# Optimization experiments

Measured on AMD Instinct MI355X. Metric: run time of the kernel, lower is better.

Reference implementation:

```python
import jax, jax.numpy as jnp
import numpy as np

EMBED_DIM = 512
NUM_HEADS = 8
HEAD_DIM = EMBED_DIM // NUM_HEADS


def setup_inputs() -> dict:
    key = jax.random.key(0)
    ks = jax.random.split(key, 6)
    B, S, D = 2, 4096, EMBED_DIM
    scale = 1.0 / np.sqrt(D)
    inputs = jax.random.normal(ks[0], (B, S, D), dtype=jnp.float32)
    Wq = jax.random.normal(ks[1], (D, D), dtype=jnp.float32) * scale
    Wk = jax.random.normal(ks[2], (D, D), dtype=jnp.float32) * scale
    Wv = jax.random.normal(ks[3], (D, D), dtype=jnp.float32) * scale
    Wo = jax.random.normal(ks[4], (D, D), dtype=jnp.float32) * scale
    zeros = jnp.zeros((D,), dtype=jnp.float32)
    return {"inputs": inputs, "Wq": Wq, "bq": zeros, "Wk": Wk, "bk": zeros,
            "Wv": Wv, "bv": zeros, "Wo": Wo, "bo": zeros}


def _split_heads(x, B, S):
    # [B,S,D] -> [B,H,S,hd]
    return x.reshape(B, S, NUM_HEADS, HEAD_DIM).transpose(0, 2, 1, 3)


def reference(inputs, Wq, bq, Wk, bk, Wv, bv, Wo, bo):
    B, S, D = inputs.shape
    q = _split_heads(inputs @ Wq + bq, B, S)
    k = _split_heads(inputs @ Wk + bk, B, S)
    v = _split_heads(inputs @ Wv + bv, B, S)
    scale = 1.0 / jnp.sqrt(jnp.asarray(HEAD_DIM, dtype=inputs.dtype))
    # full [B,H,S,S] score matrix, as in the original naive SDPA
    scores = jnp.einsum('bhqd,bhkd->bhqk', q, k) * scale
    weights = jax.nn.softmax(scores, axis=-1)
    attn = jnp.einsum('bhqk,bhkd->bhqd', weights, v)
    attn = attn.transpose(0, 2, 1, 3).reshape(B, S, D)
    return attn @ Wo + bo
```

## Files before the change

kernel.cpp:

```cpp
#include <hip/hip_runtime.h>
#include <hip/hip_bf16.h>
#include <stdint.h>


typedef __bf16 bf16x8 __attribute__((ext_vector_type(8)));
typedef float f32x4 __attribute__((ext_vector_type(4)));
typedef float f32x16 __attribute__((ext_vector_type(16)));

using as1_void = __attribute__((address_space(1))) void;
using as3_void = __attribute__((address_space(3))) void;

__device__ __forceinline__ void gload16(const void* g, void* l) {
    __builtin_amdgcn_global_load_lds((const as1_void*)g, (as3_void*)l, 16, 0, 0);
}

__device__ __forceinline__ f32x4 mfma16(bf16x8 a, bf16x8 b, f32x4 c) {
    return __builtin_amdgcn_mfma_f32_16x16x32_bf16(a, b, c, 0, 0, 0);
}

__device__ __forceinline__ f32x16 mfma32(bf16x8 a, bf16x8 b, f32x16 c) {
    return __builtin_amdgcn_mfma_f32_32x32x16_bf16(a, b, c, 0, 0, 0);
}

__device__ __forceinline__ uint32_t pkbf(float a, float b) {
    union { __hip_bfloat16 h[2]; uint32_t u; } r;
    r.h[0] = __float2bfloat16(a);
    r.h[1] = __float2bfloat16(b);
    return r.u;
}

__device__ __forceinline__ void pl32swap(uint32_t& a, uint32_t& b) {
#if __has_builtin(__builtin_amdgcn_permlane32_swap)
    typedef unsigned int uint32x2_t __attribute__((ext_vector_type(2)));
    uint32x2_t r = __builtin_amdgcn_permlane32_swap(a, b, false, false);
    a = r[0];
    b = r[1];
#else
    asm volatile("v_permlane32_swap_b32 %0, %1" : "+v"(a), "+v"(b));
#endif
}

__global__ void cvt_all(const float* __restrict__ X, __hip_bfloat16* __restrict__ Xb,
                        const float* __restrict__ w0, const float* __restrict__ w1,
                        const float* __restrict__ w2, const float* __restrict__ w3,
                        __hip_bfloat16* __restrict__ o0, __hip_bfloat16* __restrict__ o1,
                        __hip_bfloat16* __restrict__ o2, __hip_bfloat16* __restrict__ o3) {
    __shared__ float t[32][33];
    const int bid = blockIdx.x, tid = threadIdx.x;
    if (bid < 1024) {
        const float* W; __hip_bfloat16* O;
        switch (bid >> 8) {
            case 0: W = w0; O = o0; break;
            case 1: W = w1; O = o1; break;
            case 2: W = w2; O = o2; break;
            default: W = w3; O = o3; break;
        }
        int rem = bid & 255;
        int n0 = (rem & 15) * 32, k0 = (rem >> 4) * 32;
        int tx = tid & 31, ty = tid >> 5;
        for (int j = 0; j < 4; ++j)
            t[ty + 8 * j][tx] = W[(size_t)(k0 + ty + 8 * j) * 512 + n0 + tx];
        __syncthreads();
        for (int j = 0; j < 4; ++j)
            O[(size_t)(n0 + ty + 8 * j) * 512 + k0 + tx] = __float2bfloat16(t[tx][ty + 8 * j]);
    } else {
        int i = ((bid - 1024) * 256 + tid) * 4;
        float4 v = *reinterpret_cast<const float4*>(X + i);
        uint2 u;
        u.x = pkbf(v.x, v.y);
        u.y = pkbf(v.z, v.w);
        *reinterpret_cast<uint2*>(Xb + i) = u;
    }
}

__global__ __launch_bounds__(256, 2) void gemm_qkv(
    const __hip_bfloat16* __restrict__ A, const __hip_bfloat16* __restrict__ Bt,
    const float* __restrict__ bq, const float* __restrict__ bk, const float* __restrict__ bv,
    __hip_bfloat16* __restrict__ Qb, __hip_bfloat16* __restrict__ Kb,
    __hip_bfloat16* __restrict__ Vtb, float qs)
{
    const int K = 512;
    __shared__ __hip_bfloat16 Abuf[128 * 32];
    __shared__ __hip_bfloat16 Bbuf[128 * 32];
    const int tid = threadIdx.x, w = tid >> 6, lane = tid & 63;
    const int col = lane & 15, quad = lane >> 4;
    const int wr = w >> 1, wc = w & 1;
    const int tileN = blockIdx.x * 128, tileM = blockIdx.y * 128;

    f32x4 acc[4][4] = {};

    for (int k0 = 0; k0 < K; k0 += 32) {
        for (int i = 0; i < 2; ++i) {
            int g = w * 2 + i;
            int chunk = g * 64 + lane;
            int row = chunk >> 2, c8 = chunk & 3;
            gload16(A + (size_t)(tileM + row) * K + k0 + c8 * 8, Abuf + g * 512);
            gload16(Bt + (size_t)(tileN + row) * K + k0 + c8 * 8, Bbuf + g * 512);
        }
        __syncthreads();
        bf16x8 af[4], bfr[4];
        for (int mt = 0; mt < 4; ++mt)
            af[mt] = *reinterpret_cast<const bf16x8*>(Abuf + (wr * 64 + mt * 16 + col) * 32 + quad * 8);
        for (int nt = 0; nt < 4; ++nt)
            bfr[nt] = *reinterpret_cast<const bf16x8*>(Bbuf + (wc * 64 + nt * 16 + col) * 32 + quad * 8);
        for (int mt = 0; mt < 4; ++mt)
            for (int nt = 0; nt < 4; ++nt)
                acc[mt][nt] = mfma16(af[mt], bfr[nt], acc[mt][nt]);
        __syncthreads();
    }

    const int seg = (tileN + wc * 64) >> 9;
    const float* bias = (seg == 0) ? bq : (seg == 1) ? bk : bv;
    const float scale = (seg == 0) ? qs : 1.0f;
    __hip_bfloat16* outp = (seg == 0) ? Qb : (seg == 1) ? Kb : Vtb;

    for (int mt = 0; mt < 4; ++mt) {
        for (int nt = 0; nt < 4; ++nt) {
            int n = tileN + wc * 64 + nt * 16 + col;
            int nn = n & 511, h = nn >> 6, d = nn & 63;
            float bn = bias[nn];
            for (int r = 0; r < 4; ++r) {
                int m = tileM + wr * 64 + mt * 16 + quad * 4 + r;
                int b = m >> 12, s = m & 4095;
                float v = (acc[mt][nt][r] + bn) * scale;
                size_t off;
                if (seg < 2) off = (((size_t)(b * 8 + h) * 4096 + s) << 6) + d;
                else         off = (((size_t)(b * 8 + h) * 64 + d) << 12) + s;
                outp[off] = __float2bfloat16(v);
            }
        }
    }
}

__global__ __launch_bounds__(256, 2) void gemm_out(
    const __hip_bfloat16* __restrict__ A, const __hip_bfloat16* __restrict__ Bt,
    const float* __restrict__ bias, float* __restrict__ out)
{
    const int N = 512, K = 512;
    __shared__ __hip_bfloat16 Abuf[128 * 32];
    __shared__ __hip_bfloat16 Bbuf[64 * 32];
    const int tid = threadIdx.x, w = tid >> 6, lane = tid & 63;
    const int col = lane & 15, quad = lane >> 4;
    const int tileN = blockIdx.x * 64, tileM = blockIdx.y * 128;

    f32x4 acc[2][4] = {};

    for (int k0 = 0; k0 < K; k0 += 32) {
        for (int i = 0; i < 2; ++i) {
            int g = w * 2 + i;
            int chunk = g * 64 + lane;
            int row = chunk >> 2, c8 = chunk & 3;
            gload16(A + (size_t)(tileM + row) * K + k0 + c8 * 8, Abuf + g * 512);
        }
        {
            int row = tid >> 2, c8 = tid & 3;
            gload16(Bt + (size_t)(tileN + row) * K + k0 + c8 * 8, Bbuf + tid * 8);
        }
        __syncthreads();
        bf16x8 af[2], bfr[4];
        for (int mt = 0; mt < 2; ++mt)
            af[mt] = *reinterpret_cast<const bf16x8*>(Abuf + (w * 32 + mt * 16 + col) * 32 + quad * 8);
        for (int nt = 0; nt < 4; ++nt)
            bfr[nt] = *reinterpret_cast<const bf16x8*>(Bbuf + (nt * 16 + col) * 32 + quad * 8);
        for (int mt = 0; mt < 2; ++mt)
            for (int nt = 0; nt < 4; ++nt)
                acc[mt][nt] = mfma16(af[mt], bfr[nt], acc[mt][nt]);
        __syncthreads();
    }

    for (int mt = 0; mt < 2; ++mt) {
        for (int nt = 0; nt < 4; ++nt) {
            int n = tileN + nt * 16 + col;
            float bn = bias[n];
            for (int r = 0; r < 4; ++r) {
                int m = tileM + w * 32 + mt * 16 + quad * 4 + r;
                out[(size_t)m * N + n] = acc[mt][nt][r] + bn;
            }
        }
    }
}

__global__ __launch_bounds__(256, 2) void flash(
    const __hip_bfloat16* __restrict__ Q,
    const __hip_bfloat16* __restrict__ Kq,
    const __hip_bfloat16* __restrict__ Vt,
    __hip_bfloat16* __restrict__ O1,
    __hip_bfloat16* __restrict__ O2,
    float* __restrict__ Lb)
{
    __shared__ __hip_bfloat16 KT[2][4096];
    __shared__ __hip_bfloat16 VB[2][4096];

    const int bh = blockIdx.y, b = bh >> 3, hq = bh & 7;
    const int kvh = blockIdx.z;
    const int base = kvh * 32;
    const int tid = threadIdx.x, w = tid >> 6, lane = tid & 63;
    const int l31 = lane & 31, hh = lane >> 5, l7 = lane & 7;
    const int q0 = blockIdx.x * 128 + w * 32;

    const __hip_bfloat16* Qh = Q + (size_t)bh * 4096 * 64;
    const __hip_bfloat16* Kh = Kq + (size_t)bh * 4096 * 64;
    const __hip_bfloat16* Vh = Vt + (size_t)bh * 64 * 4096;

    bf16x8 aq[4];
#pragma unroll
    for (int dk = 0; dk < 4; ++dk)
        aq[dk] = *reinterpret_cast<const bf16x8*>(
            Qh + (size_t)(q0 + l31) * 64 + dk * 16 + hh * 8);

    const __hip_bfloat16* ksrc[2];
    const __hip_bfloat16* vsrc[2];
    int ldsoff[2];
#pragma unroll
    for (int i = 0; i < 2; ++i) {
        int c = i * 256 + tid;
        int row = c >> 3, s8 = (c & 7) ^ (row & 7);
        ksrc[i] = Kh + row * 64 + s8 * 8;
        vsrc[i] = Vh + (size_t)row * 4096 + s8 * 8;
        ldsoff[i] = (i * 256 + w * 64) * 8;
    }

    bf16x8 ones;
#pragma unroll
    for (int j = 0; j < 8; ++j) ones[j] = (__bf16)1.0f;

    const f32x16 z16 = {};
    f32x16 o[2] = {};
    f32x16 lacc = {};
    f32x16 sc[2][2];

    gload16(ksrc[0] + (size_t)base * 4096, &KT[0][ldsoff[0]]);
    gload16(ksrc[1] + (size_t)base * 4096, &KT[0][ldsoff[1]]);
    gload16(vsrc[0] + (size_t)base * 64, &VB[0][ldsoff[0]]);
    gload16(vsrc[1] + (size_t)base * 64, &VB[0][ldsoff[1]]);
    gload16(ksrc[0] + (size_t)(base + 1) * 4096, &KT[1][ldsoff[0]]);
    gload16(ksrc[1] + (size_t)(base + 1) * 4096, &KT[1][ldsoff[1]]);
    __syncthreads();

#define QK_STEP(KR_, SP2_)                                                      \
    _Pragma("unroll")                                                           \
    for (int kg = 0; kg < 2; ++kg) {                                            \
        _Pragma("unroll")                                                       \
        for (int dk = 0; dk < 4; ++dk) {                                        \
            bf16x8 ak = *reinterpret_cast<const bf16x8*>(                       \
                &KT[KR_][(kg * 32 + l31) * 64 + (((dk * 2 + hh) ^ l7) << 3)]);  \
            sc[SP2_][kg] = (dk == 0) ? mfma32(ak, aq[0], z16)                   \
                                     : mfma32(ak, aq[dk], sc[SP2_][kg]);        \
        }                                                                       \
    }

#define SOFTMAX_EXCHANGE(SP_)                                                   \
    uint32_t U[8][2];                                                           \
    _Pragma("unroll")                                                           \
    for (int kg = 0; kg < 2; ++kg) {                                            \
        f32x16 v = sc[SP_][kg];                                                 \
        _Pragma("unroll")                                                       \
        for (int rr = 0; rr < 4; ++rr) {                                        \
            U[kg * 4 + rr][0] = pkbf(__builtin_amdgcn_exp2f(v[rr * 4 + 0]),     \
                                     __builtin_amdgcn_exp2f(v[rr * 4 + 1]));    \
            U[kg * 4 + rr][1] = pkbf(__builtin_amdgcn_exp2f(v[rr * 4 + 2]),     \
                                     __builtin_amdgcn_exp2f(v[rr * 4 + 3]));    \
        }                                                                       \
    }                                                                           \
    bf16x8 bp[4];                                                               \
    _Pragma("unroll")                                                           \
    for (int kb = 0; kb < 4; ++kb) {                                            \
        _Pragma("unroll")                                                       \
        for (int t2 = 0; t2 < 2; ++t2)                                          \
            pl32swap(U[2 * kb][t2], U[2 * kb + 1][t2]);                         \
        union { uint32_t u[4]; bf16x8 v8; } cc;                                 \
        cc.u[0] = U[2 * kb][0];     cc.u[1] = U[2 * kb][1];                     \
        cc.u[2] = U[2 * kb + 1][0]; cc.u[3] = U[2 * kb + 1][1];                 \
        bp[kb] = cc.v8;                                                         \
    }

#define PV_STEP(VR_)                                                            \
    _Pragma("unroll")                                                           \
    for (int dg = 0; dg < 2; ++dg) {                                            \
        _Pragma("unroll")                                                       \
        for (int kb = 0; kb < 4; ++kb) {                                        \
            bf16x8 av = *reinterpret_cast<const bf16x8*>(                       \
                &VB[VR_][(dg * 32 + l31) * 64 + (((kb * 2 + hh) ^ l7) << 3)]);  \
            o[dg] = mfma32(av, bp[kb], o[dg]);                                  \
        }                                                                       \
    }                                                                           \
    _Pragma("unroll")                                                           \
    for (int kb = 0; kb < 4; ++kb) lacc = mfma32(ones, bp[kb], lacc);

    QK_STEP(0, 0)
    __syncthreads();

#define FLASH_BODY(T_, P_)                                                      \
    {                                                                           \
        const int kt_ = (T_);                                                   \
        int kk = kt_ + 2; if (kk > base + 31) kk = base + 31;                   \
        gload16(ksrc[0] + (size_t)kk * 4096, &KT[(P_)][ldsoff[0]]);             \
        gload16(ksrc[1] + (size_t)kk * 4096, &KT[(P_)][ldsoff[1]]);             \
        gload16(vsrc[0] + (size_t)(kt_ + 1) * 64, &VB[1 - (P_)][ldsoff[0]]);    \
        gload16(vsrc[1] + (size_t)(kt_ + 1) * 64, &VB[1 - (P_)][ldsoff[1]]);    \
        SOFTMAX_EXCHANGE(P_)                                                    \
        QK_STEP(1 - (P_), 1 - (P_))                                             \
        PV_STEP(P_)                                                             \
        __syncthreads();                                                        \
    }

    FLASH_BODY(base + 0, 0)
    for (int kth = 0; kth < 15; ++kth) {
        FLASH_BODY(base + 2 * kth + 1, 1)
        FLASH_BODY(base + 2 * kth + 2, 0)
    }
    {
        SOFTMAX_EXCHANGE(1)
        PV_STEP(1)
    }
#undef FLASH_BODY
#undef PV_STEP
#undef SOFTMAX_EXCHANGE
#undef QK_STEP

    {
        float l = lacc[0];
        float inv = 1.0f / l;
        int s = q0 + l31;
        __hip_bfloat16* Od = kvh ? O2 : O1;
        __hip_bfloat16* dst = Od + ((size_t)b * 4096 + s) * 512 + hq * 64;
#pragma unroll
        for (int dg = 0; dg < 2; ++dg)
#pragma unroll
            for (int rr = 0; rr < 4; ++rr) {
                uint2 u;
                u.x = pkbf(o[dg][rr * 4 + 0] * inv, o[dg][rr * 4 + 1] * inv);
                u.y = pkbf(o[dg][rr * 4 + 2] * inv, o[dg][rr * 4 + 3] * inv);
                *reinterpret_cast<uint2*>(dst + dg * 32 + rr * 8 + hh * 4) = u;
            }
        if (hh == 0)
            Lb[((size_t)kvh * 16 + bh) * 4096 + s] = l;
    }
}

__global__ __launch_bounds__(256) void merge_po(
    const __hip_bfloat16* __restrict__ O1, const __hip_bfloat16* __restrict__ O2,
    const float* __restrict__ Lb, __hip_bfloat16* __restrict__ Am)
{
    int c = blockIdx.x * 256 + threadIdx.x;
    int flat = c * 8;
    int d = flat & 511, s = (flat >> 9) & 4095, b = flat >> 21;
    int bh = b * 8 + (d >> 6);
    float l1 = Lb[(size_t)bh * 4096 + s];
    float l2 = Lb[(size_t)(16 + bh) * 4096 + s];
    float rs = 1.0f / (l1 + l2);
    float w1 = l1 * rs, w2 = l2 * rs;
    bf16x8 a = *reinterpret_cast<const bf16x8*>(O1 + flat);
    bf16x8 bb = *reinterpret_cast<const bf16x8*>(O2 + flat);
    uint2 u;
    float r0 = w1 * (float)a[0] + w2 * (float)bb[0];
    float r1 = w1 * (float)a[1] + w2 * (float)bb[1];
    float r2 = w1 * (float)a[2] + w2 * (float)bb[2];
    float r3 = w1 * (float)a[3] + w2 * (float)bb[3];
    float r4 = w1 * (float)a[4] + w2 * (float)bb[4];
    float r5 = w1 * (float)a[5] + w2 * (float)bb[5];
    float r6 = w1 * (float)a[6] + w2 * (float)bb[6];
    float r7 = w1 * (float)a[7] + w2 * (float)bb[7];
    u.x = pkbf(r0, r1);
    u.y = pkbf(r2, r3);
    uint2 v;
    v.x = pkbf(r4, r5);
    v.y = pkbf(r6, r7);
    uint4 uu = {u.x, u.y, v.x, v.y};
    *reinterpret_cast<uint4*>(Am + flat) = uu;
}

extern "C" void kernel_launch(void* const* d_in, const int* in_sizes, int n_in,
                              void* d_out, int out_size, void* d_ws, size_t ws_size,
                              hipStream_t stream) {
    const float* X  = (const float*)d_in[0];
    const float* Wq = (const float*)d_in[1];
    const float* bq = (const float*)d_in[2];
    const float* Wk = (const float*)d_in[3];
    const float* bk = (const float*)d_in[4];
    const float* Wv = (const float*)d_in[5];
    const float* bv = (const float*)d_in[6];
    const float* Wo = (const float*)d_in[7];
    const float* bo = (const float*)d_in[8];
    float* out = (float*)d_out;

    char* ws = (char*)d_ws;
    __hip_bfloat16* Xb  = (__hip_bfloat16*)(ws);
    __hip_bfloat16* Wqt = (__hip_bfloat16*)(ws + ((size_t)8 << 20));
    __hip_bfloat16* Wkt = Wqt + 512 * 512;
    __hip_bfloat16* Wvt = Wkt + 512 * 512;
    __hip_bfloat16* Wot = Wvt + 512 * 512;
    __hip_bfloat16* Qb  = (__hip_bfloat16*)(ws + ((size_t)10 << 20));
    __hip_bfloat16* Kb  = (__hip_bfloat16*)(ws + ((size_t)18 << 20));
    __hip_bfloat16* Vtb = (__hip_bfloat16*)(ws + ((size_t)26 << 20));
    __hip_bfloat16* O1  = (__hip_bfloat16*)(ws + ((size_t)34 << 20));
    __hip_bfloat16* O2  = (__hip_bfloat16*)(ws);
    __hip_bfloat16* Am  = (__hip_bfloat16*)(ws + ((size_t)10 << 20));
    float* Lb = (float*)d_out;

    cvt_all<<<5120, 256, 0, stream>>>(X, Xb, Wq, Wk, Wv, Wo, Wqt, Wkt, Wvt, Wot);

    const float qs = 0.125f * 1.4426950408889634f;
    gemm_qkv<<<dim3(12, 64), 256, 0, stream>>>(Xb, Wqt, bq, bk, bv, Qb, Kb, Vtb, qs);
    flash<<<dim3(32, 16, 2), 256, 0, stream>>>(Qb, Kb, Vtb, O1, O2, Lb);
    merge_po<<<2048, 256, 0, stream>>>(O1, O2, Lb, Am);
    gemm_out<<<dim3(8, 64), 256, 0, stream>>>(Am, Wot, bo, out);
}
```

Baseline: 221.2 us.

## Give each flash wave two query tiles and compute row sums on VALU

```diff
diff --git a/kernel.cpp b/kernel.cpp
--- a/kernel.cpp
+++ b/kernel.cpp
@@ -180,7 +180,7 @@
     }
 }
 
-__global__ __launch_bounds__(256, 2) void flash(
+__global__ __launch_bounds__(128, 2) void flash(
     const __hip_bfloat16* __restrict__ Q,
     const __hip_bfloat16* __restrict__ Kq,
     const __hip_bfloat16* __restrict__ Vt,
@@ -196,82 +196,93 @@
     const int base = kvh * 32;
     const int tid = threadIdx.x, w = tid >> 6, lane = tid & 63;
     const int l31 = lane & 31, hh = lane >> 5, l7 = lane & 7;
-    const int q0 = blockIdx.x * 128 + w * 32;
+    const int q0 = blockIdx.x * 128 + w * 64;
 
     const __hip_bfloat16* Qh = Q + (size_t)bh * 4096 * 64;
     const __hip_bfloat16* Kh = Kq + (size_t)bh * 4096 * 64;
     const __hip_bfloat16* Vh = Vt + (size_t)bh * 64 * 4096;
 
-    bf16x8 aq[4];
-#pragma unroll
-    for (int dk = 0; dk < 4; ++dk)
-        aq[dk] = *reinterpret_cast<const bf16x8*>(
-            Qh + (size_t)(q0 + l31) * 64 + dk * 16 + hh * 8);
-
-    const __hip_bfloat16* ksrc[2];
-    const __hip_bfloat16* vsrc[2];
-    int ldsoff[2];
-#pragma unroll
-    for (int i = 0; i < 2; ++i) {
-        int c = i * 256 + tid;
+    bf16x8 aq[2][4];
+#pragma unroll
+    for (int qg = 0; qg < 2; ++qg)
+#pragma unroll
+        for (int dk = 0; dk < 4; ++dk)
+            aq[qg][dk] = *reinterpret_cast<const bf16x8*>(
+                Qh + (size_t)(q0 + qg * 32 + l31) * 64 + dk * 16 + hh * 8);
+
+    const __hip_bfloat16* ksrc[4];
+    const __hip_bfloat16* vsrc[4];
+    int ldsoff[4];
+#pragma unroll
+    for (int i = 0; i < 4; ++i) {
+        int c = i * 128 + tid;
         int row = c >> 3, s8 = (c & 7) ^ (row & 7);
         ksrc[i] = Kh + row * 64 + s8 * 8;
         vsrc[i] = Vh + (size_t)row * 4096 + s8 * 8;
-        ldsoff[i] = (i * 256 + w * 64) * 8;
-    }
-
-    bf16x8 ones;
-#pragma unroll
-    for (int j = 0; j < 8; ++j) ones[j] = (__bf16)1.0f;
+        ldsoff[i] = (i * 128 + w * 64) * 8;
+    }
 
     const f32x16 z16 = {};
-    f32x16 o[2] = {};
-    f32x16 lacc = {};
+    f32x16 o[2][2] = {};
     f32x16 sc[2][2];
-
-    gload16(ksrc[0] + (size_t)base * 4096, &KT[0][ldsoff[0]]);
-    gload16(ksrc[1] + (size_t)base * 4096, &KT[0][ldsoff[1]]);
-    gload16(vsrc[0] + (size_t)base * 64, &VB[0][ldsoff[0]]);
-    gload16(vsrc[1] + (size_t)base * 64, &VB[0][ldsoff[1]]);
-    gload16(ksrc[0] + (size_t)(base + 1) * 4096, &KT[1][ldsoff[0]]);
-    gload16(ksrc[1] + (size_t)(base + 1) * 4096, &KT[1][ldsoff[1]]);
+    float ltot[2] = {0.f, 0.f};
+
+#pragma unroll
+    for (int i = 0; i < 4; ++i) gload16(ksrc[i] + (size_t)base * 4096, &KT[0][ldsoff[i]]);
+#pragma unroll
+    for (int i = 0; i < 4; ++i) gload16(vsrc[i] + (size_t)base * 64, &VB[0][ldsoff[i]]);
+#pragma unroll
+    for (int i = 0; i < 4; ++i) gload16(ksrc[i] + (size_t)(base + 1) * 4096, &KT[1][ldsoff[i]]);
     __syncthreads();
 
-#define QK_STEP(KR_, SP2_)                                                      \
+#define QK_STEP(KR_)                                                            \
     _Pragma("unroll")                                                           \
     for (int kg = 0; kg < 2; ++kg) {                                            \
         _Pragma("unroll")                                                       \
         for (int dk = 0; dk < 4; ++dk) {                                        \
             bf16x8 ak = *reinterpret_cast<const bf16x8*>(                       \
                 &KT[KR_][(kg * 32 + l31) * 64 + (((dk * 2 + hh) ^ l7) << 3)]);  \
-            sc[SP2_][kg] = (dk == 0) ? mfma32(ak, aq[0], z16)                   \
-                                     : mfma32(ak, aq[dk], sc[SP2_][kg]);        \
+            _Pragma("unroll")                                                   \
+            for (int qg = 0; qg < 2; ++qg)                                      \
+                sc[qg][kg] = (dk == 0) ? mfma32(ak, aq[qg][0], z16)             \
+                                       : mfma32(ak, aq[qg][dk], sc[qg][kg]);    \
         }                                                                       \
     }
 
-#define SOFTMAX_EXCHANGE(SP_)                                                   \
-    uint32_t U[8][2];                                                           \
+#define SOFTMAX_BP()                                                            \
+    bf16x8 bp[2][4];                                                            \
     _Pragma("unroll")                                                           \
-    for (int kg = 0; kg < 2; ++kg) {                                            \
-        f32x16 v = sc[SP_][kg];                                                 \
-        _Pragma("unroll")                                                       \
-        for (int rr = 0; rr < 4; ++rr) {                                        \
-            U[kg * 4 + rr][0] = pkbf(__builtin_amdgcn_exp2f(v[rr * 4 + 0]),     \
-                                     __builtin_amdgcn_exp2f(v[rr * 4 + 1]));    \
-            U[kg * 4 + rr][1] = pkbf(__builtin_amdgcn_exp2f(v[rr * 4 + 2]),     \
-                                     __builtin_amdgcn_exp2f(v[rr * 4 + 3]));    \
+    for (int qg = 0; qg < 2; ++qg) {                                            \
+        float ls = 0.f;                                                         \
+        uint32_t U[8][2];                                                       \
+        _Pragma("unroll")                                                       \
+        for (int kg = 0; kg < 2; ++kg) {                                        \
+            f32x16 v = sc[qg][kg];                                              \
+            _Pragma("unroll")                                                   \
+            for (int rr = 0; rr < 4; ++rr) {                                    \
+                float e0 = __builtin_amdgcn_exp2f(v[rr * 4 + 0]);               \
+                float e1 = __builtin_amdgcn_exp2f(v[rr * 4 + 1]);               \
+                float e2 = __builtin_amdgcn_exp2f(v[rr * 4 + 2]);               \
+                float e3 = __builtin_amdgcn_exp2f(v[rr * 4 + 3]);               \
+                ls += (e0 + e1) + (e2 + e3);                                    \
+                U[kg * 4 + rr][0] = pkbf(e0, e1);                               \
+                U[kg * 4 + rr][1] = pkbf(e2, e3);                               \
+            }                                                                   \
         }                                                                       \
-    }                                                                           \
-    bf16x8 bp[4];                                                               \
-    _Pragma("unroll")                                                           \
-    for (int kb = 0; kb < 4; ++kb) {                                            \
-        _Pragma("unroll")                                                       \
-        for (int t2 = 0; t2 < 2; ++t2)                                          \
-            pl32swap(U[2 * kb][t2], U[2 * kb + 1][t2]);                         \
-        union { uint32_t u[4]; bf16x8 v8; } cc;                                 \
-        cc.u[0] = U[2 * kb][0];     cc.u[1] = U[2 * kb][1];                     \
-        cc.u[2] = U[2 * kb + 1][0]; cc.u[3] = U[2 * kb + 1][1];                 \
-        bp[kb] = cc.v8;                                                         \
+        union fu_ { float f; uint32_t u; };                                     \
+        fu_ la, lb2;                                                            \
+        la.f = ls; lb2.u = la.u;                                                \
+        pl32swap(la.u, lb2.u);                                                  \
+        ltot[qg] += la.f + lb2.f;                                               \
+        _Pragma("unroll")                                                       \
+        for (int kb = 0; kb < 4; ++kb) {                                        \
+            pl32swap(U[2 * kb][0], U[2 * kb + 1][0]);                           \
+            pl32swap(U[2 * kb][1], U[2 * kb + 1][1]);                           \
+            union { uint32_t u[4]; bf16x8 v8; } cc;                             \
+            cc.u[0] = U[2 * kb][0];     cc.u[1] = U[2 * kb][1];                 \
+            cc.u[2] = U[2 * kb + 1][0]; cc.u[3] = U[2 * kb + 1][1];             \
+            bp[qg][kb] = cc.v8;                                                 \
+        }                                                                       \
     }
 
 #define PV_STEP(VR_)                                                            \
@@ -281,25 +292,27 @@
         for (int kb = 0; kb < 4; ++kb) {                                        \
             bf16x8 av = *reinterpret_cast<const bf16x8*>(                       \
                 &VB[VR_][(dg * 32 + l31) * 64 + (((kb * 2 + hh) ^ l7) << 3)]);  \
-            o[dg] = mfma32(av, bp[kb], o[dg]);                                  \
+            _Pragma("unroll")                                                   \
+            for (int qg = 0; qg < 2; ++qg)                                      \
+                o[qg][dg] = mfma32(av, bp[qg][kb], o[qg][dg]);                  \
         }                                                                       \
-    }                                                                           \
-    _Pragma("unroll")                                                           \
-    for (int kb = 0; kb < 4; ++kb) lacc = mfma32(ones, bp[kb], lacc);
-
-    QK_STEP(0, 0)
+    }
+
+    QK_STEP(0)
     __syncthreads();
 
 #define FLASH_BODY(T_, P_)                                                      \
     {                                                                           \
         const int kt_ = (T_);                                                   \
         int kk = kt_ + 2; if (kk > base + 31) kk = base + 31;                   \
-        gload16(ksrc[0] + (size_t)kk * 4096, &KT[(P_)][ldsoff[0]]);             \
-        gload16(ksrc[1] + (size_t)kk * 4096, &KT[(P_)][ldsoff[1]]);             \
-        gload16(vsrc[0] + (size_t)(kt_ + 1) * 64, &VB[1 - (P_)][ldsoff[0]]);    \
-        gload16(vsrc[1] + (size_t)(kt_ + 1) * 64, &VB[1 - (P_)][ldsoff[1]]);    \
-        SOFTMAX_EXCHANGE(P_)                                                    \
-        QK_STEP(1 - (P_), 1 - (P_))                                             \
+        _Pragma("unroll")                                                       \
+        for (int i = 0; i < 4; ++i)                                             \
+            gload16(ksrc[i] + (size_t)kk * 4096, &KT[(P_)][ldsoff[i]]);         \
+        _Pragma("unroll")                                                       \
+        for (int i = 0; i < 4; ++i)                                             \
+            gload16(vsrc[i] + (size_t)(kt_ + 1) * 64, &VB[1 - (P_)][ldsoff[i]]);\
+        SOFTMAX_BP()                                                            \
+        QK_STEP(1 - (P_))                                                       \
         PV_STEP(P_)                                                             \
         __syncthreads();                                                        \
     }
@@ -310,18 +323,19 @@
         FLASH_BODY(base + 2 * kth + 2, 0)
     }
     {
-        SOFTMAX_EXCHANGE(1)
+        SOFTMAX_BP()
         PV_STEP(1)
     }
 #undef FLASH_BODY
 #undef PV_STEP
-#undef SOFTMAX_EXCHANGE
+#undef SOFTMAX_BP
 #undef QK_STEP
 
-    {
-        float l = lacc[0];
+#pragma unroll
+    for (int qg = 0; qg < 2; ++qg) {
+        float l = ltot[qg];
         float inv = 1.0f / l;
-        int s = q0 + l31;
+        int s = q0 + qg * 32 + l31;
         __hip_bfloat16* Od = kvh ? O2 : O1;
         __hip_bfloat16* dst = Od + ((size_t)b * 4096 + s) * 512 + hq * 64;
 #pragma unroll
@@ -329,8 +343,8 @@
 #pragma unroll
             for (int rr = 0; rr < 4; ++rr) {
                 uint2 u;
-                u.x = pkbf(o[dg][rr * 4 + 0] * inv, o[dg][rr * 4 + 1] * inv);
-                u.y = pkbf(o[dg][rr * 4 + 2] * inv, o[dg][rr * 4 + 3] * inv);
+                u.x = pkbf(o[qg][dg][rr * 4 + 0] * inv, o[qg][dg][rr * 4 + 1] * inv);
+                u.y = pkbf(o[qg][dg][rr * 4 + 2] * inv, o[qg][dg][rr * 4 + 3] * inv);
                 *reinterpret_cast<uint2*>(dst + dg * 32 + rr * 8 + hh * 4) = u;
             }
         if (hh == 0)
@@ -352,7 +366,6 @@
     float w1 = l1 * rs, w2 = l2 * rs;
     bf16x8 a = *reinterpret_cast<const bf16x8*>(O1 + flat);
     bf16x8 bb = *reinterpret_cast<const bf16x8*>(O2 + flat);
-    uint2 u;
     float r0 = w1 * (float)a[0] + w2 * (float)bb[0];
     float r1 = w1 * (float)a[1] + w2 * (float)bb[1];
     float r2 = w1 * (float)a[2] + w2 * (float)bb[2];
@@ -361,12 +374,11 @@
     float r5 = w1 * (float)a[5] + w2 * (float)bb[5];
     float r6 = w1 * (float)a[6] + w2 * (float)bb[6];
     float r7 = w1 * (float)a[7] + w2 * (float)bb[7];
-    u.x = pkbf(r0, r1);
-    u.y = pkbf(r2, r3);
-    uint2 v;
-    v.x = pkbf(r4, r5);
-    v.y = pkbf(r6, r7);
-    uint4 uu = {u.x, u.y, v.x, v.y};
+    uint4 uu;
+    uu.x = pkbf(r0, r1);
+    uu.y = pkbf(r2, r3);
+    uu.z = pkbf(r4, r5);
+    uu.w = pkbf(r6, r7);
     *reinterpret_cast<uint4*>(Am + flat) = uu;
 }
 
@@ -402,7 +414,7 @@
 
     const float qs = 0.125f * 1.4426950408889634f;
     gemm_qkv<<<dim3(12, 64), 256, 0, stream>>>(Xb, Wqt, bq, bk, bv, Qb, Kb, Vtb, qs);
-    flash<<<dim3(32, 16, 2), 256, 0, stream>>>(Qb, Kb, Vtb, O1, O2, Lb);
+    flash<<<dim3(32, 16, 2), 128, 0, stream>>>(Qb, Kb, Vtb, O1, O2, Lb);
     merge_po<<<2048, 256, 0, stream>>>(O1, O2, Lb, Am);
     gemm_out<<<dim3(8, 64), 256, 0, stream>>>(Am, Wot, bo, out);
 }
```

Measured after the change: 222.6 us. Within noise of the previous version (+0.6%).
